# Kernel tuning notes

Measured on AMD Instinct MI355X. Metric: run time of the kernel, lower is better.

## Reference

```python
import jax, jax.numpy as jnp
import numpy as np

T, IN, H, R = 8192, 256, 256, 4
MEM, MVD, OUT = 256, 128, 256


def lstm_scan(xs, Wih, Whh, b, reverse=False):
    # xs: [T, F]; torch LSTM gate order i, f, g, o; b = b_ih + b_hh combined
    Hh = Whh.shape[-1]

    def step(carry, x):
        h, c = carry
        z = Wih @ x + Whh @ h + b  # [4H]
        i, f, g, o = jnp.split(z, 4)
        c = jax.nn.sigmoid(f) * c + jax.nn.sigmoid(i) * jnp.tanh(g)
        h = jax.nn.sigmoid(o) * jnp.tanh(c)
        return (h, c), h

    init = (jnp.zeros((Hh,), xs.dtype), jnp.zeros((Hh,), xs.dtype))
    _, hs = jax.lax.scan(step, init, xs, reverse=reverse)
    return hs


def bilstm(xs, Wih, Whh, b):
    # Wih: [2, 4H, F] (dir 0 = forward, dir 1 = backward)
    hf = lstm_scan(xs, Wih[0], Whh[0], b[0])
    hb = lstm_scan(xs, Wih[1], Whh[1], b[1], reverse=True)
    return jnp.concatenate([hf, hb], axis=-1)


def setup_inputs() -> dict:
    key = jax.random.key(0)
    ks = jax.random.split(key, 24)
    s = 0.05
    d = {}
    d["inputs"] = jax.random.normal(ks[0], (T, IN), jnp.float32)
    d["edges"] = jax.random.randint(ks[1], (T, 2), 0, T)
    d["memory"] = jax.random.normal(ks[2], (T, MVD), jnp.float32)
    d["Wl_ih"] = jax.random.normal(ks[3], (2, 4 * H, IN)) * s
    d["Wl_hh"] = jax.random.normal(ks[4], (2, 4 * H, H)) * s
    d["bl"] = jax.random.normal(ks[5], (2, 4 * H)) * s
    d["Wh_ih"] = jax.random.normal(ks[6], (2, 4 * H, 2 * H)) * s
    d["Wh_hh"] = jax.random.normal(ks[7], (2, 4 * H, H)) * s
    d["bh"] = jax.random.normal(ks[8], (2, 4 * H)) * s
    d["Win"] = jax.random.normal(ks[9], (H, IN)) * s
    d["bin_"] = jax.random.normal(ks[10], (H,)) * s
    d["We"] = jax.random.normal(ks[11], (R, H, 2 * H)) * s
    d["be"] = jax.random.normal(ks[12], (R, H)) * s
    d["Wn_ih"] = jax.random.normal(ks[13], (R, 4 * H, IN + H)) * s
    d["Wn_hh"] = jax.random.normal(ks[14], (R, 4 * H, H)) * s
    d["bn"] = jax.random.normal(ks[15], (R, 4 * H)) * s
    d["Wmem"] = jax.random.normal(ks[16], (MEM, H)) * s
    d["bmem"] = jax.random.normal(ks[17], (MEM,)) * s
    d["Wc_ih"] = jax.random.normal(ks[18], (4 * H, IN + 2 * H + MVD)) * s
    d["Wc_hh"] = jax.random.normal(ks[19], (4 * H, H)) * s
    d["bc"] = jax.random.normal(ks[20], (4 * H,)) * s
    d["Wout"] = jax.random.normal(ks[21], (OUT, H)) * s
    d["bout"] = jax.random.normal(ks[22], (OUT,)) * s
    return d


def reference(inputs, edges, memory, Wl_ih, Wl_hh, bl, Wh_ih, Wh_hh, bh, Win, bin_, We, be, Wn_ih, Wn_hh, bn, Wmem, bmem, Wc_ih, Wc_hh, bc, Wout, bout):
    lower = bilstm(inputs, Wl_ih, Wl_hh, bl)          # [T, 2H]
    higher = bilstm(lower, Wh_ih, Wh_hh, bh)          # [T, 2H]
    nodes = inputs @ Win.T + bin_                     # [T, H]
    for r in range(We.shape[0]):                      # fixed small relation loop
        pair = jnp.concatenate([nodes[edges[:, 0]], nodes[edges[:, 1]]], axis=1)  # [T, 2H]
        eh = pair @ We[r].T + be[r]                   # [T, H]
        nodes = lstm_scan(jnp.concatenate([inputs, eh], axis=1), Wn_ih[r], Wn_hh[r], bn[r])
    memory_vector = nodes @ Wmem.T + bmem             # [T, MEM]
    ctrl_in = jnp.concatenate([inputs, higher, memory], axis=1)  # [T, IN+2H+MVD]
    out = lstm_scan(ctrl_in, Wc_ih, Wc_hh, bc)        # [T, H]
    out = out @ Wout.T + bout                         # [T, OUT]
    return out, memory_vector
```

## Files before the change

kernel.cpp:

```cpp
#include <hip/hip_runtime.h>
#include <cstdint>


#define T_LEN 8192
#define IN_F  256
#define HID   256
#define GATE  1024
#define NREL  4
#define OUT_N 256

typedef _Float16 half2_t __attribute__((ext_vector_type(2)));

__device__ __forceinline__ float fdot2(uint32_t w, uint32_t h, float acc) {
#if __has_builtin(__builtin_amdgcn_fdot2)
  return __builtin_amdgcn_fdot2(__builtin_bit_cast(half2_t, w),
                                __builtin_bit_cast(half2_t, h), acc, false);
#else
  asm("v_dot2_f32_f16 %0, %1, %2, %0" : "+v"(acc) : "v"(w), "v"(h));
  return acc;
#endif
}

__device__ __forceinline__ float fsig(float x) { return 1.f / (1.f + __expf(-x)); }
__device__ __forceinline__ float ftanh(float x) { return 2.f / (1.f + __expf(-2.f * x)) - 1.f; }

__global__ void f2h_kernel(const float* __restrict__ in, _Float16* __restrict__ out, int n) {
  int i = blockIdx.x * blockDim.x + threadIdx.x;
  if (i < n) out[i] = (_Float16)in[i];
}

__global__ __launch_bounds__(256) void gemm_kernel(
    const float* __restrict__ A, int lda,
    const float* __restrict__ W, int ldw,
    const float* __restrict__ bias,
    const float* addC,
    float* C, int ldc, int M, int N, int K) {
  __shared__ float As[16][64];
  __shared__ float Bs[16][64];
  const int tid = threadIdx.x;
  const int tx = tid & 15, ty = tid >> 4;
  const int m0 = blockIdx.y * 64, n0 = blockIdx.x * 64;
  const int lr = tid >> 2;
  const int lc = (tid & 3) * 4;
  float acc[4][4] = {};
  for (int k0 = 0; k0 < K; k0 += 16) {
    float4 av = *(const float4*)&A[(size_t)(m0 + lr) * lda + k0 + lc];
    float4 wv = *(const float4*)&W[(size_t)(n0 + lr) * ldw + k0 + lc];
    As[lc + 0][lr] = av.x; As[lc + 1][lr] = av.y; As[lc + 2][lr] = av.z; As[lc + 3][lr] = av.w;
    Bs[lc + 0][lr] = wv.x; Bs[lc + 1][lr] = wv.y; Bs[lc + 2][lr] = wv.z; Bs[lc + 3][lr] = wv.w;
    __syncthreads();
#pragma unroll
    for (int k = 0; k < 16; ++k) {
      float a[4], b[4];
#pragma unroll
      for (int i = 0; i < 4; ++i) a[i] = As[k][ty * 4 + i];
#pragma unroll
      for (int j = 0; j < 4; ++j) b[j] = Bs[k][tx * 4 + j];
#pragma unroll
      for (int i = 0; i < 4; ++i)
#pragma unroll
        for (int j = 0; j < 4; ++j) acc[i][j] += a[i] * b[j];
    }
    __syncthreads();
  }
#pragma unroll
  for (int i = 0; i < 4; ++i) {
    int m = m0 + ty * 4 + i;
#pragma unroll
    for (int j = 0; j < 4; ++j) {
      int n = n0 + tx * 4 + j;
      float v = acc[i][j];
      if (bias) v += bias[n];
      if (addC) v += addC[(size_t)m * ldc + n];
      C[(size_t)m * ldc + n] = v;
    }
  }
}

__global__ void gather_kernel(const float* __restrict__ nodes,
                              const int* __restrict__ edges,
                              float* __restrict__ pair) {
  int t = blockIdx.x;
  int c = threadIdx.x;
  int e = edges[t * 2 + (c >> 8)];
  pair[(size_t)t * 512 + c] = nodes[(size_t)e * 256 + (c & 255)];
}

struct ScanDesc {
  const float* Xp;
  const uint32_t* W;
  float* out;
  int rev;
  int hstride;
};

__global__ __launch_bounds__(512)
__attribute__((amdgpu_waves_per_eu(2, 2)))
void lstm_scan2(ScanDesc d0, ScanDesc d1, ScanDesc d2, int T) {
  ScanDesc d;
  if (blockIdx.x == 0) d = d0;
  else if (blockIdx.x == 1) d = d1;
  else d = d2;
  const float* __restrict__ Xp = d.Xp;
  const uint32_t* __restrict__ W = d.W;
  float* __restrict__ out = d.out;
  const int rev = d.rev, hstride = d.hstride;

  const int j = threadIdx.x;
  __shared__ uint4 w_lds[2][8][512];
  __shared__ float z_lds[1024];
  __shared__ uint32_t h_lds[128];

  const uint4* wrow0 = (const uint4*)(W + (size_t)j * 128);
  const uint4* wrow1 = (const uint4*)(W + (size_t)(j + 512) * 128);
  uint4 w0[24], w1[24];
#pragma unroll
  for (int q = 0; q < 24; ++q) w0[q] = wrow0[q];
#pragma unroll
  for (int q = 0; q < 24; ++q) w1[q] = wrow1[q];
#pragma unroll
  for (int q = 0; q < 8; ++q) w_lds[0][q][j] = wrow0[24 + q];
#pragma unroll
  for (int q = 0; q < 8; ++q) w_lds[1][q][j] = wrow1[24 + q];
  if (j < 128) h_lds[j] = 0u;
  float c = 0.f;
  __syncthreads();

  const int t0 = rev ? (T - 1) : 0;
  float xp0 = Xp[(size_t)t0 * GATE + j];
  float xp1 = Xp[(size_t)t0 * GATE + j + 512];

  for (int s = 0; s < T; ++s) {
    const int t = rev ? (T - 1 - s) : s;
    float a0 = xp0, a1 = 0.f, a2 = 0.f, a3 = 0.f;
    float b0 = xp1, b1 = 0.f, b2 = 0.f, b3 = 0.f;
    {
      int sn = (s + 1 < T) ? (s + 1) : s;
      int tn = rev ? (T - 1 - sn) : sn;
      xp0 = Xp[(size_t)tn * GATE + j];
      xp1 = Xp[(size_t)tn * GATE + j + 512];
    }

    const uint4* hq = (const uint4*)h_lds;
#pragma unroll
    for (int q = 0; q < 24; ++q) {
      uint4 hv = hq[q];
      uint4 wa = w0[q], wb = w1[q];
      a0 = fdot2(wa.x, hv.x, a0); b0 = fdot2(wb.x, hv.x, b0);
      a1 = fdot2(wa.y, hv.y, a1); b1 = fdot2(wb.y, hv.y, b1);
      a2 = fdot2(wa.z, hv.z, a2); b2 = fdot2(wb.z, hv.z, b2);
      a3 = fdot2(wa.w, hv.w, a3); b3 = fdot2(wb.w, hv.w, b3);
    }
#pragma unroll
    for (int q = 0; q < 8; ++q) {
      uint4 hv = hq[24 + q];
      uint4 wa = w_lds[0][q][j], wb = w_lds[1][q][j];
      a0 = fdot2(wa.x, hv.x, a0); b0 = fdot2(wb.x, hv.x, b0);
      a1 = fdot2(wa.y, hv.y, a1); b1 = fdot2(wb.y, hv.y, b1);
      a2 = fdot2(wa.z, hv.z, a2); b2 = fdot2(wb.z, hv.z, b2);
      a3 = fdot2(wa.w, hv.w, a3); b3 = fdot2(wb.w, hv.w, b3);
    }
    z_lds[j] = (a0 + a1) + (a2 + a3);
    z_lds[j + 512] = (b0 + b1) + (b2 + b3);
    __syncthreads();

    if (j < HID) {
      float zi = z_lds[j], zf = z_lds[j + 256], zg = z_lds[j + 512], zo = z_lds[j + 768];
      float ig = fsig(zi), fg = fsig(zf), gg = ftanh(zg), og = fsig(zo);
      c = fg * c + ig * gg;
      float h = og * ftanh(c);
      out[(size_t)t * hstride + j] = h;
      ((_Float16*)h_lds)[j] = (_Float16)h;
    }
    __syncthreads();
  }
}

extern "C" void kernel_launch(void* const* d_in, const int* in_sizes, int n_in,
                              void* d_out, int out_size, void* d_ws, size_t ws_size,
                              hipStream_t stream) {
  (void)in_sizes; (void)n_in; (void)out_size; (void)ws_size;
  const float* inputs = (const float*)d_in[0];
  const int*   edges  = (const int*)d_in[1];
  const float* memory = (const float*)d_in[2];
  const float* Wl_ih  = (const float*)d_in[3];
  const float* Wl_hh  = (const float*)d_in[4];
  const float* bl     = (const float*)d_in[5];
  const float* Wh_ih  = (const float*)d_in[6];
  const float* Wh_hh  = (const float*)d_in[7];
  const float* bh     = (const float*)d_in[8];
  const float* Win    = (const float*)d_in[9];
  const float* bin_   = (const float*)d_in[10];
  const float* We     = (const float*)d_in[11];
  const float* be     = (const float*)d_in[12];
  const float* Wn_ih  = (const float*)d_in[13];
  const float* Wn_hh  = (const float*)d_in[14];
  const float* bn     = (const float*)d_in[15];
  const float* Wmem   = (const float*)d_in[16];
  const float* bmem   = (const float*)d_in[17];
  const float* Wc_ih  = (const float*)d_in[18];
  const float* Wc_hh  = (const float*)d_in[19];
  const float* bc     = (const float*)d_in[20];
  const float* Wout   = (const float*)d_in[21];
  const float* bout   = (const float*)d_in[22];

  float* out_ptr = (float*)d_out;
  float* memvec  = out_ptr + (size_t)T_LEN * OUT_N;

  char* base = (char*)d_ws;
  size_t off = 0;
  auto carve = [&](size_t nbytes) -> void* {
    void* p = base + off; off += (nbytes + 255) & ~(size_t)255; return p;
  };
  float* XpA    = (float*)carve((size_t)T_LEN * GATE * 4);
  float* XpB    = (float*)carve((size_t)T_LEN * GATE * 4);
  float* XpC    = (float*)carve((size_t)T_LEN * GATE * 4);
  float* XpN    = (float*)carve((size_t)T_LEN * GATE * 4);
  float* lower  = (float*)carve((size_t)T_LEN * 512 * 4);
  float* higher = (float*)carve((size_t)T_LEN * 512 * 4);
  float* nodesA = (float*)carve((size_t)T_LEN * 256 * 4);
  float* nodesB = (float*)carve((size_t)T_LEN * 256 * 4);
  float* pairb  = (float*)carve((size_t)T_LEN * 512 * 4);
  float* ehb    = (float*)carve((size_t)T_LEN * 256 * 4);
  float* ctrlh  = (float*)carve((size_t)T_LEN * 256 * 4);
  uint32_t* Wl16 = (uint32_t*)carve((size_t)2 * GATE * HID * 2);
  uint32_t* Wh16 = (uint32_t*)carve((size_t)2 * GATE * HID * 2);
  uint32_t* Wn16 = (uint32_t*)carve((size_t)4 * GATE * HID * 2);
  uint32_t* Wc16 = (uint32_t*)carve((size_t)1 * GATE * HID * 2);
  const size_t WMAT = (size_t)GATE * HID / 2;

  auto f2h = [&](const float* src, uint32_t* dst, int n) {
    f2h_kernel<<<(n + 255) / 256, 256, 0, stream>>>(src, (_Float16*)dst, n);
  };
  f2h(Wl_hh, Wl16, 2 * GATE * HID);
  f2h(Wh_hh, Wh16, 2 * GATE * HID);
  f2h(Wn_hh, Wn16, 4 * GATE * HID);
  f2h(Wc_hh, Wc16, 1 * GATE * HID);

  auto gemm = [&](float* C, int ldc, const float* A, int lda,
                  const float* W, int ldw, const float* bias, const float* addC,
                  int M, int N, int K) {
    dim3 g(N / 64, M / 64);
    gemm_kernel<<<g, 256, 0, stream>>>(A, lda, W, ldw, bias, addC, C, ldc, M, N, K);
  };
  auto scan3 = [&](ScanDesc a, ScanDesc b, ScanDesc c, int nblk) {
    lstm_scan2<<<nblk, 512, 0, stream>>>(a, b, c, T_LEN);
  };
  ScanDesc dummy = {};

  gemm(XpA, GATE, inputs, IN_F, Wl_ih,               IN_F, bl,        nullptr, T_LEN, GATE, IN_F);
  gemm(XpB, GATE, inputs, IN_F, Wl_ih + GATE * IN_F, IN_F, bl + GATE, nullptr, T_LEN, GATE, IN_F);
  gemm(nodesA, 256, inputs, IN_F, Win, IN_F, bin_, nullptr, T_LEN, 256, IN_F);
  gather_kernel<<<T_LEN, 512, 0, stream>>>(nodesA, edges, pairb);
  gemm(ehb, 256, pairb, 512, We + (size_t)0 * HID * 512, 512, be + 0 * HID, nullptr, T_LEN, 256, 512);
  gemm(XpN, GATE, inputs, IN_F, Wn_ih + (size_t)0 * GATE * 512,       512, bn + 0 * GATE, nullptr, T_LEN, GATE, IN_F);
  gemm(XpN, GATE, ehb,    256,  Wn_ih + (size_t)0 * GATE * 512 + 256, 512, nullptr,       XpN,     T_LEN, GATE, 256);

  scan3({XpA, Wl16,        lower,       0, 512},
        {XpB, Wl16 + WMAT, lower + 256, 1, 512},
        {XpN, Wn16,        nodesB,      0, 256}, 3);

  gemm(XpA, GATE, lower, 512, Wh_ih,              512, bh,        nullptr, T_LEN, GATE, 512);
  gemm(XpB, GATE, lower, 512, Wh_ih + GATE * 512, 512, bh + GATE, nullptr, T_LEN, GATE, 512);
  gather_kernel<<<T_LEN, 512, 0, stream>>>(nodesB, edges, pairb);
  gemm(ehb, 256, pairb, 512, We + (size_t)1 * HID * 512, 512, be + 1 * HID, nullptr, T_LEN, 256, 512);
  gemm(XpN, GATE, inputs, IN_F, Wn_ih + (size_t)1 * GATE * 512,       512, bn + 1 * GATE, nullptr, T_LEN, GATE, IN_F);
  gemm(XpN, GATE, ehb,    256,  Wn_ih + (size_t)1 * GATE * 512 + 256, 512, nullptr,       XpN,     T_LEN, GATE, 256);

  scan3({XpA, Wh16,        higher,       0, 512},
        {XpB, Wh16 + WMAT, higher + 256, 1, 512},
        {XpN, Wn16 + WMAT, nodesA,       0, 256}, 3);

  gemm(XpC, GATE, inputs, IN_F, Wc_ih,       896, bc,      nullptr, T_LEN, GATE, IN_F);
  gemm(XpC, GATE, memory, 128,  Wc_ih + 768, 896, nullptr, XpC,     T_LEN, GATE, 128);
  gemm(XpC, GATE, higher, 512,  Wc_ih + 256, 896, nullptr, XpC,     T_LEN, GATE, 512);
  gather_kernel<<<T_LEN, 512, 0, stream>>>(nodesA, edges, pairb);
  gemm(ehb, 256, pairb, 512, We + (size_t)2 * HID * 512, 512, be + 2 * HID, nullptr, T_LEN, 256, 512);
  gemm(XpN, GATE, inputs, IN_F, Wn_ih + (size_t)2 * GATE * 512,       512, bn + 2 * GATE, nullptr, T_LEN, GATE, IN_F);
  gemm(XpN, GATE, ehb,    256,  Wn_ih + (size_t)2 * GATE * 512 + 256, 512, nullptr,       XpN,     T_LEN, GATE, 256);

  scan3({XpN, Wn16 + 2 * WMAT, nodesB, 0, 256},
        {XpC, Wc16,            ctrlh,  0, 256}, dummy, 2);

  gather_kernel<<<T_LEN, 512, 0, stream>>>(nodesB, edges, pairb);
  gemm(ehb, 256, pairb, 512, We + (size_t)3 * HID * 512, 512, be + 3 * HID, nullptr, T_LEN, 256, 512);
  gemm(XpN, GATE, inputs, IN_F, Wn_ih + (size_t)3 * GATE * 512,       512, bn + 3 * GATE, nullptr, T_LEN, GATE, IN_F);
  gemm(XpN, GATE, ehb,    256,  Wn_ih + (size_t)3 * GATE * 512 + 256, 512, nullptr,       XpN,     T_LEN, GATE, 256);

  scan3({XpN, Wn16 + 3 * WMAT, nodesA, 0, 256}, dummy, dummy, 1);

  gemm(memvec,  256, nodesA, 256, Wmem, HID, bmem, nullptr, T_LEN, 256, HID);
  gemm(out_ptr, 256, ctrlh,  256, Wout, HID, bout, nullptr, T_LEN, 256, HID);
}
```

Baseline: 62.14 ms.

## Use MFMA matrix cores for LSTM recurrent matvec with pre-swizzled weight fragments

The recurrent scan kernel now computes W_hh·h with 16x16x32 f16 MFMA instructions in 4 waves, not per-thread dot2 over 512 threads. Weights are pre-swizzled into MFMA fragment layout by a new prep kernel. Half of each matrix's fragments are pinned in AGPRs, and the rest are streamed from global/L2 every step with inline-asm loads. The h vector is broadcast as the B operand, which wastes 15 of 16 columns, and the per-step global weight reloads add memory latency to the serial chain.

```diff
diff --git a/kernel.cpp b/kernel.cpp
--- a/kernel.cpp
+++ b/kernel.cpp
@@ -9,25 +9,17 @@
 #define NREL  4
 #define OUT_N 256
 
-typedef _Float16 half2_t __attribute__((ext_vector_type(2)));
-
-__device__ __forceinline__ float fdot2(uint32_t w, uint32_t h, float acc) {
-#if __has_builtin(__builtin_amdgcn_fdot2)
-  return __builtin_amdgcn_fdot2(__builtin_bit_cast(half2_t, w),
-                                __builtin_bit_cast(half2_t, h), acc, false);
-#else
-  asm("v_dot2_f32_f16 %0, %1, %2, %0" : "+v"(acc) : "v"(w), "v"(h));
-  return acc;
-#endif
+typedef _Float16 f16x8 __attribute__((ext_vector_type(8)));
+typedef float    f32x4 __attribute__((ext_vector_type(4)));
+typedef uint32_t u32x4 __attribute__((ext_vector_type(4)));
+
+__device__ __forceinline__ f32x4 mfma16(u32x4 a, u32x4 b, f32x4 c) {
+  return __builtin_amdgcn_mfma_f32_16x16x32_f16(
+      __builtin_bit_cast(f16x8, a), __builtin_bit_cast(f16x8, b), c, 0, 0, 0);
 }
 
 __device__ __forceinline__ float fsig(float x) { return 1.f / (1.f + __expf(-x)); }
 __device__ __forceinline__ float ftanh(float x) { return 2.f / (1.f + __expf(-2.f * x)) - 1.f; }
-
-__global__ void f2h_kernel(const float* __restrict__ in, _Float16* __restrict__ out, int n) {
-  int i = blockIdx.x * blockDim.x + threadIdx.x;
-  if (i < n) out[i] = (_Float16)in[i];
-}
 
 __global__ __launch_bounds__(256) void gemm_kernel(
     const float* __restrict__ A, int lda,
@@ -55,11 +47,11 @@
 #pragma unroll
       for (int i = 0; i < 4; ++i) a[i] = As[k][ty * 4 + i];
 #pragma unroll
-      for (int j = 0; j < 4; ++j) b[j] = Bs[k][tx * 4 + j];
+      for (int jj = 0; jj < 4; ++jj) b[jj] = Bs[k][tx * 4 + jj];
 #pragma unroll
       for (int i = 0; i < 4; ++i)
 #pragma unroll
-        for (int j = 0; j < 4; ++j) acc[i][j] += a[i] * b[j];
+        for (int jj = 0; jj < 4; ++jj) acc[i][jj] += a[i] * b[jj];
     }
     __syncthreads();
   }
@@ -67,9 +59,9 @@
   for (int i = 0; i < 4; ++i) {
     int m = m0 + ty * 4 + i;
 #pragma unroll
-    for (int j = 0; j < 4; ++j) {
-      int n = n0 + tx * 4 + j;
-      float v = acc[i][j];
+    for (int jj = 0; jj < 4; ++jj) {
+      int n = n0 + tx * 4 + jj;
+      float v = acc[i][jj];
       if (bias) v += bias[n];
       if (addC) v += addC[(size_t)m * ldc + n];
       C[(size_t)m * ldc + n] = v;
@@ -86,91 +78,182 @@
   pair[(size_t)t * 512 + c] = nodes[(size_t)e * 256 + (c & 255)];
 }
 
+struct PrepSrcs { const float* p[9]; };
+
+__global__ __launch_bounds__(256) void prep_frags(PrepSrcs s, u32x4* __restrict__ outAll) {
+  int id = blockIdx.x * 256 + threadIdx.x;
+  int mat = id >> 15;
+  int r   = id & 32767;
+  int l   = r & 63;
+  int kc  = (r >> 6) & 7;
+  int rt  = (r >> 9) & 15;
+  int w   = r >> 13;
+  const float* W = s.p[mat];
+  int row = w * 256 + rt * 16 + (l & 15);
+  int kb  = kc * 32 + ((l >> 4) << 3);
+  const float* src = W + (size_t)row * 256 + kb;
+  uint32_t dw[4];
+#pragma unroll
+  for (int i = 0; i < 4; ++i) {
+    uint16_t lo = __builtin_bit_cast(uint16_t, (_Float16)src[2 * i]);
+    uint16_t hi = __builtin_bit_cast(uint16_t, (_Float16)src[2 * i + 1]);
+    dw[i] = (uint32_t)lo | ((uint32_t)hi << 16);
+  }
+  u32x4 v = {dw[0], dw[1], dw[2], dw[3]};
+  outAll[id] = v;
+}
+
 struct ScanDesc {
   const float* Xp;
-  const uint32_t* W;
+  const u32x4* Wf;
   float* out;
   int rev;
   int hstride;
 };
 
-__global__ __launch_bounds__(512)
-__attribute__((amdgpu_waves_per_eu(2, 2)))
-void lstm_scan2(ScanDesc d0, ScanDesc d1, ScanDesc d2, int T) {
+#define GLD(dst, base, OFF) \
+  asm volatile("global_load_dwordx4 %0, %1, off offset:" OFF : "=v"(dst) : "v"(base))
+
+#define SLOAD8(S, BA, BB) \
+  GLD(S##_0, BA, "0"); GLD(S##_1, BA, "1024"); GLD(S##_2, BA, "2048"); GLD(S##_3, BA, "3072"); \
+  GLD(S##_4, BB, "0"); GLD(S##_5, BB, "1024"); GLD(S##_6, BB, "2048"); GLD(S##_7, BB, "3072");
+
+__global__ __launch_bounds__(256)
+__attribute__((amdgpu_waves_per_eu(1, 1)))
+void lstm_scan_mfma(ScanDesc d0, ScanDesc d1, ScanDesc d2, int T) {
   ScanDesc d;
   if (blockIdx.x == 0) d = d0;
   else if (blockIdx.x == 1) d = d1;
   else d = d2;
   const float* __restrict__ Xp = d.Xp;
-  const uint32_t* __restrict__ W = d.W;
   float* __restrict__ out = d.out;
   const int rev = d.rev, hstride = d.hstride;
 
   const int j = threadIdx.x;
-  __shared__ uint4 w_lds[2][8][512];
-  __shared__ float z_lds[1024];
-  __shared__ uint32_t h_lds[128];
-
-  const uint4* wrow0 = (const uint4*)(W + (size_t)j * 128);
-  const uint4* wrow1 = (const uint4*)(W + (size_t)(j + 512) * 128);
-  uint4 w0[24], w1[24];
-#pragma unroll
-  for (int q = 0; q < 24; ++q) w0[q] = wrow0[q];
-#pragma unroll
-  for (int q = 0; q < 24; ++q) w1[q] = wrow1[q];
-#pragma unroll
-  for (int q = 0; q < 8; ++q) w_lds[0][q][j] = wrow0[24 + q];
-#pragma unroll
-  for (int q = 0; q < 8; ++q) w_lds[1][q][j] = wrow1[24 + q];
-  if (j < 128) h_lds[j] = 0u;
+  const int w = j >> 6, l = j & 63;
+
+  __shared__ __align__(16) float z_sh[1024];
+  __shared__ __align__(16) _Float16 h_sh[256];
+
+  const u32x4* fb = d.Wf + (size_t)w * 8192 + l;
+
+#define AG_DECL(rt, kc) u32x4 A##rt##_##kc = fb[((rt) * 8 + (kc)) * 64];
+#define AG_ROW(rt) AG_DECL(rt,0) AG_DECL(rt,1) AG_DECL(rt,2) AG_DECL(rt,3) \
+                   AG_DECL(rt,4) AG_DECL(rt,5) AG_DECL(rt,6) AG_DECL(rt,7)
+  AG_ROW(0) AG_ROW(1) AG_ROW(2) AG_ROW(3) AG_ROW(4) AG_ROW(5) AG_ROW(6) AG_ROW(7)
+#define AG_PIN(rt, kc) asm volatile("" : "+a"(A##rt##_##kc));
+#define AG_PINR(rt) AG_PIN(rt,0) AG_PIN(rt,1) AG_PIN(rt,2) AG_PIN(rt,3) \
+                    AG_PIN(rt,4) AG_PIN(rt,5) AG_PIN(rt,6) AG_PIN(rt,7)
+  AG_PINR(0) AG_PINR(1) AG_PINR(2) AG_PINR(3) AG_PINR(4) AG_PINR(5) AG_PINR(6) AG_PINR(7)
+
+  const u32x4* sb8a  = fb + 8  * 512; const u32x4* sb8b  = sb8a  + 256;
+  const u32x4* sb9a  = fb + 9  * 512; const u32x4* sb9b  = sb9a  + 256;
+  const u32x4* sb10a = fb + 10 * 512; const u32x4* sb10b = sb10a + 256;
+  const u32x4* sb11a = fb + 11 * 512; const u32x4* sb11b = sb11a + 256;
+  const u32x4* sb12a = fb + 12 * 512; const u32x4* sb12b = sb12a + 256;
+  const u32x4* sb13a = fb + 13 * 512; const u32x4* sb13b = sb13a + 256;
+  const u32x4* sb14a = fb + 14 * 512; const u32x4* sb14b = sb14a + 256;
+  const u32x4* sb15a = fb + 15 * 512; const u32x4* sb15b = sb15a + 256;
+
+  if (j < 128) ((uint32_t*)h_sh)[j] = 0u;
   float c = 0.f;
+  const int t0 = rev ? (T - 1) : 0;
+  float xpi = Xp[(size_t)t0 * GATE + j];
+  float xpf = Xp[(size_t)t0 * GATE + j + 256];
+  float xpg = Xp[(size_t)t0 * GATE + j + 512];
+  float xpo = Xp[(size_t)t0 * GATE + j + 768];
   __syncthreads();
-
-  const int t0 = rev ? (T - 1) : 0;
-  float xp0 = Xp[(size_t)t0 * GATE + j];
-  float xp1 = Xp[(size_t)t0 * GATE + j + 512];
 
   for (int s = 0; s < T; ++s) {
     const int t = rev ? (T - 1 - s) : s;
-    float a0 = xp0, a1 = 0.f, a2 = 0.f, a3 = 0.f;
-    float b0 = xp1, b1 = 0.f, b2 = 0.f, b3 = 0.f;
+
+    u32x4 S0_0, S0_1, S0_2, S0_3, S0_4, S0_5, S0_6, S0_7;
+    u32x4 S1_0, S1_1, S1_2, S1_3, S1_4, S1_5, S1_6, S1_7;
+    u32x4 S2_0, S2_1, S2_2, S2_3, S2_4, S2_5, S2_6, S2_7;
+    u32x4 S3_0, S3_1, S3_2, S3_3, S3_4, S3_5, S3_6, S3_7;
+
+    SLOAD8(S0, sb8a,  sb8b)
+    SLOAD8(S1, sb9a,  sb9b)
+    SLOAD8(S2, sb10a, sb10b)
+    SLOAD8(S3, sb11a, sb11b)
+
+    const char* hbase = (const char*)h_sh + ((l >> 4) << 4);
+    u32x4 hb0 = *(const u32x4*)(hbase + 0);
+    u32x4 hb1 = *(const u32x4*)(hbase + 64);
+    u32x4 hb2 = *(const u32x4*)(hbase + 128);
+    u32x4 hb3 = *(const u32x4*)(hbase + 192);
+    u32x4 hb4 = *(const u32x4*)(hbase + 256);
+    u32x4 hb5 = *(const u32x4*)(hbase + 320);
+    u32x4 hb6 = *(const u32x4*)(hbase + 384);
+    u32x4 hb7 = *(const u32x4*)(hbase + 448);
+
+    f32x4 acc0 = {0.f,0.f,0.f,0.f}, acc1 = {0.f,0.f,0.f,0.f};
+    f32x4 acc2 = {0.f,0.f,0.f,0.f}, acc3 = {0.f,0.f,0.f,0.f};
+    f32x4 acc4 = {0.f,0.f,0.f,0.f}, acc5 = {0.f,0.f,0.f,0.f};
+    f32x4 acc6 = {0.f,0.f,0.f,0.f}, acc7 = {0.f,0.f,0.f,0.f};
+#define MFK(kc) \
+    acc0 = mfma16(A0_##kc, hb##kc, acc0); acc1 = mfma16(A1_##kc, hb##kc, acc1); \
+    acc2 = mfma16(A2_##kc, hb##kc, acc2); acc3 = mfma16(A3_##kc, hb##kc, acc3); \
+    acc4 = mfma16(A4_##kc, hb##kc, acc4); acc5 = mfma16(A5_##kc, hb##kc, acc5); \
+    acc6 = mfma16(A6_##kc, hb##kc, acc6); acc7 = mfma16(A7_##kc, hb##kc, acc7);
+    MFK(0) MFK(1) MFK(2) MFK(3) MFK(4) MFK(5) MFK(6) MFK(7)
+#undef MFK
+
+    const int zb = (w << 8) + ((l >> 4) << 2);
+#define ZW(rt) if ((l & 15) == 0) *(f32x4*)&z_sh[zb + (rt) * 16] = acc##rt;
+    ZW(0) ZW(1) ZW(2) ZW(3) ZW(4) ZW(5) ZW(6) ZW(7)
+#undef ZW
+
+    asm volatile("s_waitcnt vmcnt(0)" ::: "memory");
+    __builtin_amdgcn_sched_barrier(0);
+    f32x4 sacc0 = {0.f,0.f,0.f,0.f}, sacc1 = {0.f,0.f,0.f,0.f};
+    f32x4 sacc2 = {0.f,0.f,0.f,0.f}, sacc3 = {0.f,0.f,0.f,0.f};
+#define SMK(kc) \
+    sacc0 = mfma16(S0_##kc, hb##kc, sacc0); sacc1 = mfma16(S1_##kc, hb##kc, sacc1); \
+    sacc2 = mfma16(S2_##kc, hb##kc, sacc2); sacc3 = mfma16(S3_##kc, hb##kc, sacc3);
+    SMK(0) SMK(1) SMK(2) SMK(3) SMK(4) SMK(5) SMK(6) SMK(7)
+    if ((l & 15) == 0) {
+      *(f32x4*)&z_sh[zb + 8  * 16] = sacc0;
+      *(f32x4*)&z_sh[zb + 9  * 16] = sacc1;
+      *(f32x4*)&z_sh[zb + 10 * 16] = sacc2;
+      *(f32x4*)&z_sh[zb + 11 * 16] = sacc3;
+    }
+
+    SLOAD8(S0, sb12a, sb12b)
+    SLOAD8(S1, sb13a, sb13b)
+    SLOAD8(S2, sb14a, sb14b)
+    SLOAD8(S3, sb15a, sb15b)
+    asm volatile("s_waitcnt vmcnt(0)" ::: "memory");
+    __builtin_amdgcn_sched_barrier(0);
+    sacc0 = (f32x4){0.f,0.f,0.f,0.f}; sacc1 = (f32x4){0.f,0.f,0.f,0.f};
+    sacc2 = (f32x4){0.f,0.f,0.f,0.f}; sacc3 = (f32x4){0.f,0.f,0.f,0.f};
+    SMK(0) SMK(1) SMK(2) SMK(3) SMK(4) SMK(5) SMK(6) SMK(7)
+#undef SMK
+    if ((l & 15) == 0) {
+      *(f32x4*)&z_sh[zb + 12 * 16] = sacc0;
+      *(f32x4*)&z_sh[zb + 13 * 16] = sacc1;
+      *(f32x4*)&z_sh[zb + 14 * 16] = sacc2;
+      *(f32x4*)&z_sh[zb + 15 * 16] = sacc3;
+    }
+
+    __syncthreads();
+
     {
-      int sn = (s + 1 < T) ? (s + 1) : s;
-      int tn = rev ? (T - 1 - sn) : sn;
-      xp0 = Xp[(size_t)tn * GATE + j];
-      xp1 = Xp[(size_t)tn * GATE + j + 512];
-    }
-
-    const uint4* hq = (const uint4*)h_lds;
-#pragma unroll
-    for (int q = 0; q < 24; ++q) {
-      uint4 hv = hq[q];
-      uint4 wa = w0[q], wb = w1[q];
-      a0 = fdot2(wa.x, hv.x, a0); b0 = fdot2(wb.x, hv.x, b0);
-      a1 = fdot2(wa.y, hv.y, a1); b1 = fdot2(wb.y, hv.y, b1);
-      a2 = fdot2(wa.z, hv.z, a2); b2 = fdot2(wb.z, hv.z, b2);
-      a3 = fdot2(wa.w, hv.w, a3); b3 = fdot2(wb.w, hv.w, b3);
-    }
-#pragma unroll
-    for (int q = 0; q < 8; ++q) {
-      uint4 hv = hq[24 + q];
-      uint4 wa = w_lds[0][q][j], wb = w_lds[1][q][j];
-      a0 = fdot2(wa.x, hv.x, a0); b0 = fdot2(wb.x, hv.x, b0);
-      a1 = fdot2(wa.y, hv.y, a1); b1 = fdot2(wb.y, hv.y, b1);
-      a2 = fdot2(wa.z, hv.z, a2); b2 = fdot2(wb.z, hv.z, b2);
-      a3 = fdot2(wa.w, hv.w, a3); b3 = fdot2(wb.w, hv.w, b3);
-    }
-    z_lds[j] = (a0 + a1) + (a2 + a3);
-    z_lds[j + 512] = (b0 + b1) + (b2 + b3);
-    __syncthreads();
-
-    if (j < HID) {
-      float zi = z_lds[j], zf = z_lds[j + 256], zg = z_lds[j + 512], zo = z_lds[j + 768];
+      float zi = z_sh[j]       + xpi;
+      float zf = z_sh[j + 256] + xpf;
+      float zg = z_sh[j + 512] + xpg;
+      float zo = z_sh[j + 768] + xpo;
       float ig = fsig(zi), fg = fsig(zf), gg = ftanh(zg), og = fsig(zo);
       c = fg * c + ig * gg;
       float h = og * ftanh(c);
       out[(size_t)t * hstride + j] = h;
-      ((_Float16*)h_lds)[j] = (_Float16)h;
+      h_sh[j] = (_Float16)h;
+      int sn = (s + 1 < T) ? (s + 1) : s;
+      int tn = rev ? (T - 1 - sn) : sn;
+      xpi = Xp[(size_t)tn * GATE + j];
+      xpf = Xp[(size_t)tn * GATE + j + 256];
+      xpg = Xp[(size_t)tn * GATE + j + 512];
+      xpo = Xp[(size_t)tn * GATE + j + 768];
     }
     __syncthreads();
   }
@@ -223,19 +306,16 @@
   float* pairb  = (float*)carve((size_t)T_LEN * 512 * 4);
   float* ehb    = (float*)carve((size_t)T_LEN * 256 * 4);
   float* ctrlh  = (float*)carve((size_t)T_LEN * 256 * 4);
-  uint32_t* Wl16 = (uint32_t*)carve((size_t)2 * GATE * HID * 2);
-  uint32_t* Wh16 = (uint32_t*)carve((size_t)2 * GATE * HID * 2);
-  uint32_t* Wn16 = (uint32_t*)carve((size_t)4 * GATE * HID * 2);
-  uint32_t* Wc16 = (uint32_t*)carve((size_t)1 * GATE * HID * 2);
-  const size_t WMAT = (size_t)GATE * HID / 2;
-
-  auto f2h = [&](const float* src, uint32_t* dst, int n) {
-    f2h_kernel<<<(n + 255) / 256, 256, 0, stream>>>(src, (_Float16*)dst, n);
-  };
-  f2h(Wl_hh, Wl16, 2 * GATE * HID);
-  f2h(Wh_hh, Wh16, 2 * GATE * HID);
-  f2h(Wn_hh, Wn16, 4 * GATE * HID);
-  f2h(Wc_hh, Wc16, 1 * GATE * HID);
+  u32x4* Wf_all = (u32x4*)carve((size_t)9 * 32768 * 16);
+
+  PrepSrcs ps;
+  ps.p[0] = Wl_hh;            ps.p[1] = Wl_hh + 262144;
+  ps.p[2] = Wh_hh;            ps.p[3] = Wh_hh + 262144;
+  ps.p[4] = Wn_hh;            ps.p[5] = Wn_hh + 262144;
+  ps.p[6] = Wn_hh + 524288;   ps.p[7] = Wn_hh + 786432;
+  ps.p[8] = Wc_hh;
+  prep_frags<<<9 * 32768 / 256, 256, 0, stream>>>(ps, Wf_all);
+  auto Wf = [&](int m) { return (const u32x4*)(Wf_all + (size_t)m * 32768); };
 
   auto gemm = [&](float* C, int ldc, const float* A, int lda,
                   const float* W, int ldw, const float* bias, const float* addC,
@@ -244,7 +324,7 @@
     gemm_kernel<<<g, 256, 0, stream>>>(A, lda, W, ldw, bias, addC, C, ldc, M, N, K);
   };
   auto scan3 = [&](ScanDesc a, ScanDesc b, ScanDesc c, int nblk) {
-    lstm_scan2<<<nblk, 512, 0, stream>>>(a, b, c, T_LEN);
+    lstm_scan_mfma<<<nblk, 256, 0, stream>>>(a, b, c, T_LEN);
   };
   ScanDesc dummy = {};
 
@@ -256,9 +336,9 @@
   gemm(XpN, GATE, inputs, IN_F, Wn_ih + (size_t)0 * GATE * 512,       512, bn + 0 * GATE, nullptr, T_LEN, GATE, IN_F);
   gemm(XpN, GATE, ehb,    256,  Wn_ih + (size_t)0 * GATE * 512 + 256, 512, nullptr,       XpN,     T_LEN, GATE, 256);
 
-  scan3({XpA, Wl16,        lower,       0, 512},
-        {XpB, Wl16 + WMAT, lower + 256, 1, 512},
-        {XpN, Wn16,        nodesB,      0, 256}, 3);
+  scan3({XpA, Wf(0), lower,       0, 512},
+        {XpB, Wf(1), lower + 256, 1, 512},
+        {XpN, Wf(4), nodesB,      0, 256}, 3);
 
   gemm(XpA, GATE, lower, 512, Wh_ih,              512, bh,        nullptr, T_LEN, GATE, 512);
   gemm(XpB, GATE, lower, 512, Wh_ih + GATE * 512, 512, bh + GATE, nullptr, T_LEN, GATE, 512);
@@ -267,9 +347,9 @@
   gemm(XpN, GATE, inputs, IN_F, Wn_ih + (size_t)1 * GATE * 512,       512, bn + 1 * GATE, nullptr, T_LEN, GATE, IN_F);
   gemm(XpN, GATE, ehb,    256,  Wn_ih + (size_t)1 * GATE * 512 + 256, 512, nullptr,       XpN,     T_LEN, GATE, 256);
 
-  scan3({XpA, Wh16,        higher,       0, 512},
-        {XpB, Wh16 + WMAT, higher + 256, 1, 512},
-        {XpN, Wn16 + WMAT, nodesA,       0, 256}, 3);
+  scan3({XpA, Wf(2), higher,       0, 512},
+        {XpB, Wf(3), higher + 256, 1, 512},
+        {XpN, Wf(5), nodesA,       0, 256}, 3);
 
   gemm(XpC, GATE, inputs, IN_F, Wc_ih,       896, bc,      nullptr, T_LEN, GATE, IN_F);
   gemm(XpC, GATE, memory, 128,  Wc_ih + 768, 896, nullptr, XpC,     T_LEN, GATE, 128);
@@ -279,15 +359,15 @@
   gemm(XpN, GATE, inputs, IN_F, Wn_ih + (size_t)2 * GATE * 512,       512, bn + 2 * GATE, nullptr, T_LEN, GATE, IN_F);
   gemm(XpN, GATE, ehb,    256,  Wn_ih + (size_t)2 * GATE * 512 + 256, 512, nullptr,       XpN,     T_LEN, GATE, 256);
 
-  scan3({XpN, Wn16 + 2 * WMAT, nodesB, 0, 256},
-        {XpC, Wc16,            ctrlh,  0, 256}, dummy, 2);
+  scan3({XpN, Wf(6), nodesB, 0, 256},
+        {XpC, Wf(8), ctrlh,  0, 256}, dummy, 2);
 
   gather_kernel<<<T_LEN, 512, 0, stream>>>(nodesB, edges, pairb);
   gemm(ehb, 256, pairb, 512, We + (size_t)3 * HID * 512, 512, be + 3 * HID, nullptr, T_LEN, 256, 512);
   gemm(XpN, GATE, inputs, IN_F, Wn_ih + (size_t)3 * GATE * 512,       512, bn + 3 * GATE, nullptr, T_LEN, GATE, IN_F);
   gemm(XpN, GATE, ehb,    256,  Wn_ih + (size_t)3 * GATE * 512 + 256, 512, nullptr,       XpN,     T_LEN, GATE, 256);
 
-  scan3({XpN, Wn16 + 3 * WMAT, nodesA, 0, 256}, dummy, dummy, 1);
+  scan3({XpN, Wf(7), nodesA, 0, 256}, dummy, dummy, 1);
 
   gemm(memvec,  256, nodesA, 256, Wmem, HID, bmem, nullptr, T_LEN, 256, HID);
   gemm(out_ptr, 256, ctrlh,  256, Wout, HID, bout, nullptr, T_LEN, 256, HID);
```

Result: slower. 90.71 ms (+46.0%).
